# Performance work log

Hardware: AMD Instinct MI355X
Metric: run time of the kernel (lower is better)

The kernel has to match this reference:

```python
import jax, jax.numpy as jnp
import numpy as np
from jax import lax

B, T, C = 128, 2048, 128


def setup_inputs() -> dict:
    key = jax.random.key(0)
    k1, k2 = jax.random.split(key)
    inputs = jax.random.normal(k1, (B, T, C), dtype=jnp.float32)
    transitions = jax.random.normal(k2, (C, C), dtype=jnp.float32)
    return {"inputs": inputs, "transitions": transitions}


def _viterbi_decode(potentials, transitions):
    """Max-plus Viterbi decode, full sequence lengths.
    potentials: [B, T, C], transitions: [C, C] -> tags [B, T] int32."""
    def fwd_step(alpha, pot_t):
        # alpha: [B, C] best score ending in each tag at t-1
        scores = alpha[:, :, None] + transitions[None, :, :]  # [B, C_prev, C_cur]
        best_prev = jnp.max(scores, axis=1)                    # [B, C]
        bp = jnp.argmax(scores, axis=1).astype(jnp.int32)      # [B, C] backpointers
        return best_prev + pot_t, bp

    alpha0 = potentials[:, 0]                                  # [B, C]
    pots_rest = jnp.swapaxes(potentials[:, 1:], 0, 1)          # [T-1, B, C]
    alpha_T, bps = lax.scan(fwd_step, alpha0, pots_rest)

    last_tag = jnp.argmax(alpha_T, axis=-1).astype(jnp.int32)  # [B]

    def back_step(tag, bp_t):
        prev = jnp.take_along_axis(bp_t, tag[:, None], axis=1)[:, 0]
        return prev, prev

    # reverse scan over backpointers; outputs stacked in original time order
    _, tags_prefix = lax.scan(back_step, last_tag, bps, reverse=True)  # [T-1, B]
    tags = jnp.concatenate([tags_prefix, last_tag[None, :]], axis=0)   # [T, B]
    return jnp.swapaxes(tags, 0, 1)                                    # [B, T]


def reference(inputs, transitions):
    # CRF.call at inference: viterbi decode, tags cast to input dtype
    tags = _viterbi_decode(inputs, transitions)
    return tags.astype(inputs.dtype)
```

## Files before the change

### kernel.cpp

```cpp
#include <hip/hip_runtime.h>
#include <cstdint>
#include <cstddef>

#define B_DIM 128
#define T_LEN 2048
#define C_DIM 128
#define NSTEP (T_LEN - 1)
#define NS4   512

#define FSKEW(x) ((x) + 8 * ((x) >> 5))

#define LDS_BARRIER() asm volatile("s_waitcnt lgkmcnt(0)\n\ts_barrier" ::: "memory")

#define TR_LIST(X) \
    X(0)  X(1)  X(2)  X(3)  X(4)  X(5)  X(6)  X(7)  \
    X(8)  X(9)  X(10) X(11) X(12) X(13) X(14) X(15) \
    X(16) X(17) X(18) X(19) X(20) X(21) X(22) X(23) \
    X(24) X(25) X(26) X(27) X(28) X(29) X(30) X(31)

template <int CTRL>
__device__ __forceinline__ float dppf(float x)
{
    return __int_as_float(__builtin_amdgcn_update_dpp(
        0, __float_as_int(x), CTRL, 0xF, 0xF, true));
}

__device__ __forceinline__ float max32(const float s[32])
{
    float u[11];
#pragma unroll
    for (int p = 0; p < 10; ++p)
        u[p] = fmaxf(fmaxf(s[3 * p], s[3 * p + 1]), s[3 * p + 2]);
    u[10] = fmaxf(s[30], s[31]);
    const float w0 = fmaxf(fmaxf(u[0], u[1]), u[2]);
    const float w1 = fmaxf(fmaxf(u[3], u[4]), u[5]);
    const float w2 = fmaxf(fmaxf(u[6], u[7]), u[8]);
    const float w3 = fmaxf(u[9], u[10]);
    return fmaxf(fmaxf(w0, w1), fmaxf(w2, w3));
}

__global__ __launch_bounds__(512)
__attribute__((amdgpu_waves_per_eu(2, 2)))
void viterbi_fwd_a(
    const float* __restrict__ pot,
    const float* __restrict__ trans,
    float* __restrict__ vstarG,
    int* __restrict__ lastTag)
{
    const int b   = blockIdx.x;
    const int tid = threadIdx.x;
    const int w   = tid >> 6;
    const int l   = tid & 63;
    const int d   = l & 3;
    const int j   = 16 * w + (l >> 2);
    const int fj  = FSKEW(j);
    const int ib  = 32 * d;

    __shared__ __align__(16) float alphabuf[2][160];

#define DECL_TR(K) const float tr_##K = trans[(ib + (K)) * C_DIM + j];
    TR_LIST(DECL_TR)
#undef DECL_TR

    const float* potb = pot + (size_t)b * T_LEN * C_DIM;
    float* vG = vstarG + (size_t)b * NSTEP * C_DIM;

    if (tid < C_DIM) alphabuf[1][FSKEW(tid)] = potb[tid];

    float pq0 = potb[1 * C_DIM + j];
    float pq1 = potb[2 * C_DIM + j];
    float pq2 = potb[3 * C_DIM + j];
    float pq3 = potb[4 * C_DIM + j];
    __syncthreads();

#define ADD_TR(K) s_[K] = a_[K] + tr_##K;

#define STEP_A(T_, PQ_)                                                       \
    {                                                                         \
        const float* ac_ = &alphabuf[(T_) & 1][40 * d];                       \
        float a_[32];                                                         \
        _Pragma("unroll")                                                     \
        for (int e_ = 0; e_ < 8; ++e_)                                        \
            *(float4*)&a_[4 * e_] = *(const float4*)&ac_[4 * e_];             \
        float s_[32];                                                         \
        TR_LIST(ADD_TR)                                                       \
        float v_ = max32(s_);                                                 \
        v_ = fmaxf(v_, dppf<0xB1>(v_));                                       \
        v_ = fmaxf(v_, dppf<0x4E>(v_));                                       \
        const float av_ = v_ + (PQ_);                                         \
        alphabuf[((T_) + 1) & 1][fj] = av_;                                   \
        vG[(size_t)((T_) - 1) * C_DIM + j] = v_;                              \
        const int tn_ = ((T_) + 4 < T_LEN) ? ((T_) + 4) : (T_LEN - 1);        \
        PQ_ = potb[tn_ * C_DIM + j];         \
        LDS_BARRIER();                                                        \
    }

    for (int t = 1; t < 2045; t += 4) {
        STEP_A(t + 0, pq0)
        STEP_A(t + 1, pq1)
        STEP_A(t + 2, pq2)
        STEP_A(t + 3, pq3)
    }
    STEP_A(2045, pq0)
    STEP_A(2046, pq1)
    STEP_A(2047, pq2)
#undef STEP_A
#undef ADD_TR

    if (tid < 64) {
        const float* af = alphabuf[0];
        const float v0 = af[FSKEW(tid)];
        const float v1 = af[FSKEW(tid + 64)];
        float v = v0; int x = tid;
        if (v1 > v0) { v = v1; x = tid + 64; }
#pragma unroll
        for (int mk = 1; mk < 64; mk <<= 1) {
            const float pv = __shfl_xor(v, mk);
            const int   px = __shfl_xor(x, mk);
            if (pv > v || (pv == v && px < x)) { v = pv; x = px; }
        }
        if (tid == 0) lastTag[b] = x;
    }
}

__global__ __launch_bounds__(64, 1) void viterbi_bwd_v(
    const float* __restrict__ pot,
    const float* __restrict__ vstarG,
    const float* __restrict__ trans,
    const int* __restrict__ lastTag,
    float* __restrict__ out)
{
    const int b = blockIdx.x;
    const int l = threadIdx.x;
    float* outb = out + (size_t)b * T_LEN;
    const float* potb = pot + (size_t)b * T_LEN * C_DIM;
    const float* vbse = vstarG + (size_t)b * NSTEP * C_DIM;

    __shared__ float Tl[C_DIM][C_DIM];
    for (int k = l; k < C_DIM * C_DIM; k += 64) {
        const int i = k >> 7;
        const int jj = k & 127;
        Tl[i][jj ^ (i & 31)] = trans[k];
    }

    float pa0, pb0, pa1, pb1, pa2, pb2, pa3, pb3, pa4, pb4, pa5, pb5;
    float va0, vb0, va1, vb1, va2, vb2, va3, vb3, va4, vb4, va5, vb5;
    auto ld = [&](int r, float& pa, float& pb, float& va, float& vb) {
        const int rr = (r > 0) ? r : 0;
        pa = potb[(size_t)rr * C_DIM + l];
        pb = potb[(size_t)rr * C_DIM + l + 64];
        va = vbse[(size_t)rr * C_DIM + l];
        vb = vbse[(size_t)rr * C_DIM + l + 64];
    };
    ld(2046, pa0, pb0, va0, vb0);
    ld(2045, pa1, pb1, va1, vb1);
    ld(2044, pa2, pb2, va2, vb2);
    ld(2043, pa3, pb3, va3, vb3);
    ld(2042, pa4, pb4, va4, vb4);
    ld(2041, pa5, pb5, va5, vb5);

    int cur = lastTag[b];
    outb[T_LEN - 1] = (float)cur;
    __syncthreads();

    for (int r = NSTEP - 1; r >= 1; --r) {
        const int cl = cur & 63;
        const float rl0 = __int_as_float(
            __builtin_amdgcn_readlane(__float_as_int(va0), cl));
        const float rl1 = __int_as_float(
            __builtin_amdgcn_readlane(__float_as_int(vb0), cl));
        const float smax = (cur & 64) ? rl1 : rl0;
        const float a0 = pa0 + va1;
        const float a1 = pb0 + vb1;
        const int sw = cur ^ (l & 31);
        const float c0 = Tl[l][sw];
        const float c1 = Tl[l + 64][sw];
        const float s0 = a0 + c0;
        const float s1 = a1 + c1;
        const unsigned long long m0 = __ballot(s0 == smax);
        const unsigned long long m1 = __ballot(s1 == smax);
        cur = m0 ? (__ffsll(m0) - 1) : (64 + __ffsll(m1) - 1);
        outb[r] = (float)cur;
        pa0 = pa1; pb0 = pb1; va0 = va1; vb0 = vb1;
        pa1 = pa2; pb1 = pb2; va1 = va2; vb1 = vb2;
        pa2 = pa3; pb2 = pb3; va2 = va3; vb2 = vb3;
        pa3 = pa4; pb3 = pb4; va3 = va4; vb3 = vb4;
        pa4 = pa5; pb4 = pb5; va4 = va5; vb4 = vb5;
        ld(r - 6, pa5, pb5, va5, vb5);
    }
    {
        const int cl = cur & 63;
        const float rl0 = __int_as_float(
            __builtin_amdgcn_readlane(__float_as_int(va0), cl));
        const float rl1 = __int_as_float(
            __builtin_amdgcn_readlane(__float_as_int(vb0), cl));
        const float smax = (cur & 64) ? rl1 : rl0;
        const float a0 = pa0;
        const float a1 = pb0;
        const int sw = cur ^ (l & 31);
        const float s0 = a0 + Tl[l][sw];
        const float s1 = a1 + Tl[l + 64][sw];
        const unsigned long long m0 = __ballot(s0 == smax);
        const unsigned long long m1 = __ballot(s1 == smax);
        cur = m0 ? (__ffsll(m0) - 1) : (64 + __ffsll(m1) - 1);
        outb[0] = (float)cur;
    }
}

__global__ __launch_bounds__(512)
__attribute__((amdgpu_waves_per_eu(2, 2)))
void viterbi_fwd(
    const float* __restrict__ pot,
    const float* __restrict__ trans,
    unsigned* __restrict__ bp4,
    int* __restrict__ lastTag)
{
    const int b   = blockIdx.x;
    const int tid = threadIdx.x;
    const int w   = tid >> 6;
    const int l   = tid & 63;
    const int d   = l & 3;
    const int j   = 16 * w + (l >> 2);
    const int fj  = FSKEW(j);
    const int ib  = 32 * d;

    __shared__ __align__(16) float alphabuf[2][160];

#define DECL_TR(K) float tr_##K = trans[(ib + (K)) * C_DIM + j];
    TR_LIST(DECL_TR)
#undef DECL_TR

    const float* potb = pot + (size_t)b * T_LEN * C_DIM;

    if (tid < C_DIM) alphabuf[1][FSKEW(tid)] = potb[tid];

    float pq0 = 0.f, pq1 = 0.f, pq2 = 0.f, pq3 = 0.f;
    if (d == 0) {
        pq0 = potb[1 * C_DIM + j];
        pq1 = potb[2 * C_DIM + j];
        pq2 = potb[3 * C_DIM + j];
        pq3 = potb[4 * C_DIM + j];
    }
    unsigned pack = 0;
    __syncthreads();

#define ADD_TR(K) s_[K] = a_[K] + tr_##K;

#define STEP(T_, C_, PQ_)                                                     \
    {                                                                         \
        const float* ac_ = &alphabuf[(T_) & 1][40 * d];                       \
        float a_[32];                                                         \
        _Pragma("unroll")                                                     \
        for (int e_ = 0; e_ < 8; ++e_)                                        \
            *(float4*)&a_[4 * e_] = *(const float4*)&ac_[4 * e_];             \
        float s_[32];                                                         \
        TR_LIST(ADD_TR)                                                       \
        float v16_[16]; int x16_[16];                                         \
        _Pragma("unroll")                                                     \
        for (int p_ = 0; p_ < 16; ++p_) {                                     \
            const bool g_ = s_[2 * p_ + 1] > s_[2 * p_];                      \
            v16_[p_] = g_ ? s_[2 * p_ + 1] : s_[2 * p_];                      \
            x16_[p_] = g_ ? 2 * p_ + 1 : 2 * p_;                              \
        }                                                                     \
        float v8_[8]; int x8_[8];                                             \
        _Pragma("unroll")                                                     \
        for (int p_ = 0; p_ < 8; ++p_) {                                      \
            const bool g_ = v16_[2 * p_ + 1] > v16_[2 * p_];                  \
            v8_[p_] = g_ ? v16_[2 * p_ + 1] : v16_[2 * p_];                   \
            x8_[p_] = g_ ? x16_[2 * p_ + 1] : x16_[2 * p_];                   \
        }                                                                     \
        float v4_[4]; int x4_[4];                                             \
        _Pragma("unroll")                                                     \
        for (int p_ = 0; p_ < 4; ++p_) {                                      \
            const bool g_ = v8_[2 * p_ + 1] > v8_[2 * p_];                    \
            v4_[p_] = g_ ? v8_[2 * p_ + 1] : v8_[2 * p_];                     \
            x4_[p_] = g_ ? x8_[2 * p_ + 1] : x8_[2 * p_];                     \
        }                                                                     \
        float v2_[2]; int x2_[2];                                             \
        _Pragma("unroll")                                                     \
        for (int p_ = 0; p_ < 2; ++p_) {                                      \
            const bool g_ = v4_[2 * p_ + 1] > v4_[2 * p_];                    \
            v2_[p_] = g_ ? v4_[2 * p_ + 1] : v4_[2 * p_];                     \
            x2_[p_] = g_ ? x4_[2 * p_ + 1] : x4_[2 * p_];                     \
        }                                                                     \
        const bool gf_ = v2_[1] > v2_[0];                                     \
        float v_ = gf_ ? v2_[1] : v2_[0];                                     \
        int   x_ = ib + (gf_ ? x2_[1] : x2_[0]);                              \
        {                                                                     \
            const float pv_ = __int_as_float(__builtin_amdgcn_update_dpp(     \
                0, __float_as_int(v_), 0xB1, 0xF, 0xF, true));                \
            const int   px_ = __builtin_amdgcn_update_dpp(                    \
                0, x_, 0xB1, 0xF, 0xF, true);                                 \
            const bool  pl_ = d & 1;                                          \
            const bool  tk_ = (pv_ > v_) || (pl_ && (pv_ == v_));             \
            if (tk_) { v_ = pv_; x_ = px_; }                                  \
        }                                                                     \
        {                                                                     \
            const float pv_ = __int_as_float(__builtin_amdgcn_update_dpp(     \
                0, __float_as_int(v_), 0x4E, 0xF, 0xF, true));                \
            const int   px_ = __builtin_amdgcn_update_dpp(                    \
                0, x_, 0x4E, 0xF, 0xF, true);                                 \
            const bool  pl_ = (d >> 1) & 1;                                   \
            const bool  tk_ = (pv_ > v_) || (pl_ && (pv_ == v_));             \
            if (tk_) { v_ = pv_; x_ = px_; }                                  \
        }                                                                     \
        if (d == 0) {                                                         \
            alphabuf[((T_) + 1) & 1][fj] = v_ + (PQ_);                        \
            pack |= (unsigned)x_ << (8 * (C_));                               \
            if ((C_) == 3) {                                                  \
                bp4[((size_t)(((T_) - 1) >> 2) * B_DIM + b) * C_DIM + j] =    \
                    pack;                                                     \
                pack = 0;                                                     \
            }                                                                 \
            if ((T_) + 4 < T_LEN) PQ_ = potb[((T_) + 4) * C_DIM + j];         \
        }                                                                     \
        LDS_BARRIER();                                                        \
    }

    for (int t = 1; t < 2045; t += 4) {
        STEP(t + 0, 0, pq0)
        STEP(t + 1, 1, pq1)
        STEP(t + 2, 2, pq2)
        STEP(t + 3, 3, pq3)
    }
    STEP(2045, 0, pq0)
    STEP(2046, 1, pq1)
    STEP(2047, 2, pq2)
    if (d == 0)
        bp4[((size_t)511 * B_DIM + b) * C_DIM + j] = pack;
#undef STEP
#undef ADD_TR

    if (tid < 64) {
        const float* af = alphabuf[0];
        const float v0 = af[FSKEW(tid)];
        const float v1 = af[FSKEW(tid + 64)];
        float v = v0; int x = tid;
        if (v1 > v0) { v = v1; x = tid + 64; }
#pragma unroll
        for (int mk = 1; mk < 64; mk <<= 1) {
            const float pv = __shfl_xor(v, mk);
            const int   px = __shfl_xor(x, mk);
            if (pv > v || (pv == v && px < x)) { v = pv; x = px; }
        }
        if (tid == 0) lastTag[b] = x;
    }
}

__global__ __launch_bounds__(64, 1) void viterbi_bwd(
    const unsigned* __restrict__ bp4,
    const int* __restrict__ lastTag,
    float* __restrict__ out)
{
    const int b = blockIdx.x;
    const int l = threadIdx.x;
    float* outb = out + (size_t)b * T_LEN;

    unsigned qa0 = 0, qb0 = 0, qa1 = 0, qb1 = 0,
             qa2 = 0, qb2 = 0, qa3 = 0, qb3 = 0;

    auto ld = [&](int s4, unsigned& A, unsigned& B) {
        if (s4 >= 0) {
            const unsigned* r = bp4 + ((size_t)s4 * B_DIM + b) * C_DIM;
            A = r[l];
            B = r[l + 64];
        }
    };
    ld(511, qa0, qb0);
    ld(510, qa1, qb1);
    ld(509, qa2, qb2);
    ld(508, qa3, qb3);

    int cur = lastTag[b];

    auto ext = [&](unsigned rA, unsigned rB, int c, int byte) -> int {
        const int addr = (c & 63) << 2;
        const int vA = __builtin_amdgcn_ds_bpermute(addr, (int)rA);
        const int vB = __builtin_amdgcn_ds_bpermute(addr, (int)rB);
        const int v = (c & 64) ? vB : vA;
        return (v >> (byte * 8)) & 0xFF;
    };

    {
        const unsigned rA = qa0, rB = qb0;
        const float t3 = (float)cur;
        cur = ext(rA, rB, cur, 2); const float t2 = (float)cur;
        cur = ext(rA, rB, cur, 1); const float t1 = (float)cur;
        cur = ext(rA, rB, cur, 0); const float t0 = (float)cur;
        if (l == 0) *(float4*)(outb + 4 * 511) = make_float4(t0, t1, t2, t3);
        qa0 = qa1; qb0 = qb1; qa1 = qa2; qb1 = qb2; qa2 = qa3; qb2 = qb3;
        ld(507, qa3, qb3);
    }

    for (int s4 = 510; s4 >= 0; --s4) {
        const unsigned rA = qa0, rB = qb0;
        cur = ext(rA, rB, cur, 3); const float t3 = (float)cur;
        cur = ext(rA, rB, cur, 2); const float t2 = (float)cur;
        cur = ext(rA, rB, cur, 1); const float t1 = (float)cur;
        cur = ext(rA, rB, cur, 0); const float t0 = (float)cur;
        if (l == 0) *(float4*)(outb + 4 * s4) = make_float4(t0, t1, t2, t3);
        qa0 = qa1; qb0 = qb1; qa1 = qa2; qb1 = qb2; qa2 = qa3; qb2 = qb3;
        ld(s4 - 4, qa3, qb3);
    }
}

extern "C" void kernel_launch(void* const* d_in, const int* in_sizes, int n_in,
                              void* d_out, int out_size, void* d_ws, size_t ws_size,
                              hipStream_t stream)
{
    const float* pot   = (const float*)d_in[0];
    const float* trans = (const float*)d_in[1];
    float* out = (float*)d_out;

    const size_t vstarBytes = (size_t)B_DIM * NSTEP * C_DIM * sizeof(float);

    if (ws_size >= vstarBytes + 512) {
        float* vstarG = (float*)d_ws;
        int* lastTag  = (int*)((char*)d_ws + vstarBytes);
        viterbi_fwd_a<<<B_DIM, 512, 0, stream>>>(pot, trans, vstarG, lastTag);
        viterbi_bwd_v<<<B_DIM, 64, 0, stream>>>(pot, vstarG, trans, lastTag, out);
    } else {
        unsigned* bp4 = (unsigned*)d_ws;
        int* lastTag  = (int*)((char*)d_ws + (size_t)NS4 * B_DIM * C_DIM * 4);
        viterbi_fwd<<<B_DIM, 512, 0, stream>>>(pot, trans, bp4, lastTag);
        viterbi_bwd<<<B_DIM, 64, 0, stream>>>(bp4, lastTag, out);
    }
}
```

Measured before the change: 1.097 ms.

## Split forward Viterbi max over 8 lanes per tag using 1024-thread blocks

The forward max-plus kernel now assigns 8 lanes per output tag instead of 4, so each lane handles 16 predecessor scores rather than 32. The block grows to 1024 threads, with a new LDS skew layout and a third DPP step (row half mirror) to finish the 8-lane max reduction. The aim is to shorten the serial per-timestep critical path of adds and max operations. In exchange, each per-step barrier now synchronises 16 waves instead of 8, and the kernel drops the waves-per-EU hint.

```diff
diff --git a/kernel.cpp b/kernel.cpp
--- a/kernel.cpp
+++ b/kernel.cpp
@@ -9,8 +9,13 @@
 #define NS4   512
 
 #define FSKEW(x) ((x) + 8 * ((x) >> 5))
+#define FSKEW16(x) ((x) + 4 * ((x) >> 4))
 
 #define LDS_BARRIER() asm volatile("s_waitcnt lgkmcnt(0)\n\ts_barrier" ::: "memory")
+
+#define TR16_LIST(X) \
+    X(0)  X(1)  X(2)  X(3)  X(4)  X(5)  X(6)  X(7)  \
+    X(8)  X(9)  X(10) X(11) X(12) X(13) X(14) X(15)
 
 #define TR_LIST(X) \
     X(0)  X(1)  X(2)  X(3)  X(4)  X(5)  X(6)  X(7)  \
@@ -23,6 +28,17 @@
 {
     return __int_as_float(__builtin_amdgcn_update_dpp(
         0, __float_as_int(x), CTRL, 0xF, 0xF, true));
+}
+
+__device__ __forceinline__ float max16(const float s[16])
+{
+    const float u0 = fmaxf(fmaxf(s[0], s[1]), s[2]);
+    const float u1 = fmaxf(fmaxf(s[3], s[4]), s[5]);
+    const float u2 = fmaxf(fmaxf(s[6], s[7]), s[8]);
+    const float u3 = fmaxf(fmaxf(s[9], s[10]), s[11]);
+    const float u4 = fmaxf(s[12], s[13]);
+    const float u5 = fmaxf(s[14], s[15]);
+    return fmaxf(fmaxf(fmaxf(u0, u1), fmaxf(u2, u3)), fmaxf(u4, u5));
 }
 
 __device__ __forceinline__ float max32(const float s[32])
@@ -39,9 +55,8 @@
     return fmaxf(fmaxf(w0, w1), fmaxf(w2, w3));
 }
 
-__global__ __launch_bounds__(512)
-__attribute__((amdgpu_waves_per_eu(2, 2)))
-void viterbi_fwd_a(
+__global__ __launch_bounds__(1024)
+void viterbi_fwd_a16(
     const float* __restrict__ pot,
     const float* __restrict__ trans,
     float* __restrict__ vstarG,
@@ -51,21 +66,22 @@
     const int tid = threadIdx.x;
     const int w   = tid >> 6;
     const int l   = tid & 63;
-    const int d   = l & 3;
-    const int j   = 16 * w + (l >> 2);
-    const int fj  = FSKEW(j);
-    const int ib  = 32 * d;
+    const int d3  = l & 7;
+    const int m   = l >> 3;
+    const int j   = 8 * w + m;
+    const int fj  = FSKEW16(j);
+    const int ib  = 16 * d3;
 
     __shared__ __align__(16) float alphabuf[2][160];
 
 #define DECL_TR(K) const float tr_##K = trans[(ib + (K)) * C_DIM + j];
-    TR_LIST(DECL_TR)
+    TR16_LIST(DECL_TR)
 #undef DECL_TR
 
     const float* potb = pot + (size_t)b * T_LEN * C_DIM;
     float* vG = vstarG + (size_t)b * NSTEP * C_DIM;
 
-    if (tid < C_DIM) alphabuf[1][FSKEW(tid)] = potb[tid];
+    if (tid < C_DIM) alphabuf[1][FSKEW16(tid)] = potb[tid];
 
     float pq0 = potb[1 * C_DIM + j];
     float pq1 = potb[2 * C_DIM + j];
@@ -77,16 +93,17 @@
 
 #define STEP_A(T_, PQ_)                                                       \
     {                                                                         \
-        const float* ac_ = &alphabuf[(T_) & 1][40 * d];                       \
-        float a_[32];                                                         \
-        _Pragma("unroll")                                                     \
-        for (int e_ = 0; e_ < 8; ++e_)                                        \
+        const float* ac_ = &alphabuf[(T_) & 1][20 * d3];                      \
+        float a_[16];                                                         \
+        _Pragma("unroll")                                                     \
+        for (int e_ = 0; e_ < 4; ++e_)                                        \
             *(float4*)&a_[4 * e_] = *(const float4*)&ac_[4 * e_];             \
-        float s_[32];                                                         \
-        TR_LIST(ADD_TR)                                                       \
-        float v_ = max32(s_);                                                 \
-        v_ = fmaxf(v_, dppf<0xB1>(v_));                                       \
-        v_ = fmaxf(v_, dppf<0x4E>(v_));                                       \
+        float s_[16];                                                         \
+        TR16_LIST(ADD_TR)                                                     \
+        float v_ = max16(s_);                                                 \
+        v_ = fmaxf(v_, dppf<0xB1>(v_));                             \
+        v_ = fmaxf(v_, dppf<0x4E>(v_));                             \
+        v_ = fmaxf(v_, dppf<0x141>(v_));          \
         const float av_ = v_ + (PQ_);                                         \
         alphabuf[((T_) + 1) & 1][fj] = av_;                                   \
         vG[(size_t)((T_) - 1) * C_DIM + j] = v_;                              \
@@ -109,8 +126,8 @@
 
     if (tid < 64) {
         const float* af = alphabuf[0];
-        const float v0 = af[FSKEW(tid)];
-        const float v1 = af[FSKEW(tid + 64)];
+        const float v0 = af[FSKEW16(tid)];
+        const float v1 = af[FSKEW16(tid + 64)];
         float v = v0; int x = tid;
         if (v1 > v0) { v = v1; x = tid + 64; }
 #pragma unroll
@@ -417,7 +434,7 @@
     if (ws_size >= vstarBytes + 512) {
         float* vstarG = (float*)d_ws;
         int* lastTag  = (int*)((char*)d_ws + vstarBytes);
-        viterbi_fwd_a<<<B_DIM, 512, 0, stream>>>(pot, trans, vstarG, lastTag);
+        viterbi_fwd_a16<<<B_DIM, 1024, 0, stream>>>(pot, trans, vstarG, lastTag);
         viterbi_bwd_v<<<B_DIM, 64, 0, stream>>>(pot, vstarG, trans, lastTag, out);
     } else {
         unsigned* bp4 = (unsigned*)d_ws;
```

Measured after the change: 1.104 ms. Within noise of the previous version (+0.7%).
